# Kernel optimization log

Measured on AMD Instinct MI355X. Metric: run time of the kernel, lower is better.

The kernel has to match this reference:

```python
import jax, jax.numpy as jnp
import numpy as np

B = 16384
MOTION = 128      # motion_size
USED = 3          # used_motions
LAT = 32          # latent_size
H1 = 512
H2 = 512
MOE = 8
IN = MOTION * (USED - 1) + LAT  # 288 (used_angles = 0)


def setup_inputs() -> dict:
    key = jax.random.key(0)
    ks = jax.random.split(key, 14)
    s = 0.02
    return {
        "motions": jax.random.normal(ks[0], (B, MOTION * (USED - 1)), jnp.float32),
        "z": jax.random.normal(ks[1], (B, LAT), jnp.float32),
        # gate MLP params
        "gw1": jax.random.normal(ks[2], (IN, H1), jnp.float32) * s,
        "gb1": jnp.zeros((H1,), jnp.float32),
        "gw2": jax.random.normal(ks[3], (H1, H2), jnp.float32) * s,
        "gb2": jnp.zeros((H2,), jnp.float32),
        "gw3": jax.random.normal(ks[4], (H2, MOE), jnp.float32) * s,
        "gb3": jnp.zeros((MOE,), jnp.float32),
        # stacked expert params: layer k weight [MOE, in_k, out_k]
        "W1": jax.random.normal(ks[5], (MOE, IN, H1), jnp.float32) * s,
        "b1": jnp.zeros((MOE, H1), jnp.float32),
        "W2": jax.random.normal(ks[6], (MOE, H1 + LAT, H2), jnp.float32) * s,
        "b2": jnp.zeros((MOE, H2), jnp.float32),
        "W3": jax.random.normal(ks[7], (MOE, H2 + LAT, MOTION), jnp.float32) * s,
        "b3": jnp.zeros((MOE, MOTION), jnp.float32),
    }


def reference(motions, z, gw1, gb1, gw2, gb2, gw3, gb3, W1, b1, W2, b2, W3, b3):
    # used_angles == 0 -> angles is empty; input = concat([motions, z])
    x = jnp.concatenate([motions, z], axis=1)            # [B, IN]

    # gate: 3-layer ELU MLP -> per-expert blend weights [B, MOE]
    para = jax.nn.elu(x @ gw1 + gb1)
    para = jax.nn.elu(para @ gw2 + gb2)
    para = jax.nn.elu(para @ gw3 + gb3)

    # all experts batched via stacked weights (replaces Python loop)
    zb = jnp.broadcast_to(z[None], (MOE, B, LAT))        # z re-concatenated per layer
    h = jax.nn.elu(jnp.einsum('bi,eio->ebo', x, W1) + b1[:, None, :])              # [E,B,H1]
    h = jax.nn.elu(jnp.einsum('ebi,eio->ebo', jnp.concatenate([h, zb], -1), W2)
                   + b2[:, None, :])                                               # [E,B,H2]
    h = jax.nn.elu(jnp.einsum('ebi,eio->ebo', jnp.concatenate([h, zb], -1), W3)
                   + b3[:, None, :])                                               # [E,B,M]

    # gated combine, then divide by Frobenius norm of the whole gate matrix
    out = jnp.einsum('be,ebm->bm', para, h)              # [B, MOTION]
    out = out / jnp.linalg.norm(para)
    return jax.nn.sigmoid(out)
```

## Files before the change

kernel.cpp:

```cpp
#include <hip/hip_runtime.h>


typedef __attribute__((ext_vector_type(8))) short bf16x8;
typedef __attribute__((ext_vector_type(4))) float f32x4;
#define MFMA(a, b, c) __builtin_amdgcn_mfma_f32_16x16x32_bf16(a, b, c, 0, 0, 0)

#define STRIDE 552

__device__ __forceinline__ float elu_f(float x) { return x > 0.f ? x : (__expf(x) - 1.f); }

__device__ __forceinline__ ushort f2bf(float f) {
    union { float f; unsigned u; } v; v.f = f;
    unsigned r = v.u + 0x7fffu + ((v.u >> 16) & 1u);
    return (ushort)(r >> 16);
}
__device__ __forceinline__ float bf2f(ushort u) {
    union { unsigned u; float f; } v; v.u = ((unsigned)u) << 16;
    return v.f;
}
__device__ __forceinline__ bf16x8 ldg8(const ushort* p) { return *(const bf16x8*)p; }

__global__ void prep_xz(const float* __restrict__ motions, const float* __restrict__ z,
                        ushort* __restrict__ xz) {
    int i = blockIdx.x * 256 + threadIdx.x;
    int r = i / 72, c = i % 72;
    float4 v = (c < 64) ? ((const float4*)motions)[r * 64 + c]
                        : ((const float4*)z)[r * 8 + (c - 64)];
    ushort4 o;
    o.x = f2bf(v.x); o.y = f2bf(v.y); o.z = f2bf(v.z); o.w = f2bf(v.w);
    *(ushort4*)(xz + (size_t)r * 288 + c * 4) = o;
}

__global__ void prep_transpose(const float* __restrict__ in, ushort* __restrict__ out,
                               int K, int N) {
    __shared__ float tile[32][33];
    const int e = blockIdx.z;
    const float* inp = in + (size_t)e * K * N;
    ushort* outp = out + (size_t)e * N * K;
    const int k0 = blockIdx.x * 32, n0 = blockIdx.y * 32;
    const int tx = threadIdx.x, ty = threadIdx.y;
    #pragma unroll
    for (int i = 0; i < 4; ++i)
        tile[ty + i * 8][tx] = inp[(size_t)(k0 + ty + i * 8) * N + n0 + tx];
    __syncthreads();
    #pragma unroll
    for (int i = 0; i < 4; ++i)
        outp[(size_t)(n0 + ty + i * 8) * K + k0 + tx] = f2bf(tile[tx][ty + i * 8]);
}

__device__ __forceinline__ void layer_x288(
    int e, const ushort* __restrict__ Wall, const float* __restrict__ ball,
    const ushort* __restrict__ xrow, ushort* hdst, int n0, int lr, int lk)
{
    const ushort* Wt = Wall + (size_t)e * 512 * 288;
    f32x4 acc[4][2] = {};
    bf16x8 bc[2], bn[2];
    #pragma unroll
    for (int nf = 0; nf < 2; ++nf)
        bc[nf] = ldg8(Wt + (size_t)(n0 + nf * 16 + lr) * 288 + lk * 8);
    for (int ks = 0; ks < 9; ++ks) {
        if (ks < 8) {
            #pragma unroll
            for (int nf = 0; nf < 2; ++nf)
                bn[nf] = ldg8(Wt + (size_t)(n0 + nf * 16 + lr) * 288 + (ks + 1) * 32 + lk * 8);
        }
        bf16x8 a[4];
        #pragma unroll
        for (int mf = 0; mf < 4; ++mf)
            a[mf] = ldg8(xrow + (size_t)(mf * 16 + lr) * 288 + ks * 32 + lk * 8);
        #pragma unroll
        for (int mf = 0; mf < 4; ++mf) {
            acc[mf][0] = MFMA(bc[0], a[mf], acc[mf][0]);
            acc[mf][1] = MFMA(bc[1], a[mf], acc[mf][1]);
        }
        bc[0] = bn[0]; bc[1] = bn[1];
    }
    #pragma unroll
    for (int nf = 0; nf < 2; ++nf) {
        const int nb = n0 + nf * 16 + lk * 4;
        const float4 bb = *(const float4*)&ball[e * 512 + nb];
        #pragma unroll
        for (int mf = 0; mf < 4; ++mf) {
            const int row = mf * 16 + lr;
            ushort4 o;
            o.x = f2bf(elu_f(acc[mf][nf][0] + bb.x));
            o.y = f2bf(elu_f(acc[mf][nf][1] + bb.y));
            o.z = f2bf(elu_f(acc[mf][nf][2] + bb.z));
            o.w = f2bf(elu_f(acc[mf][nf][3] + bb.w));
            *(ushort4*)&hdst[row * STRIDE + nb] = o;
        }
    }
}

__device__ __forceinline__ void layer_h544(
    int e, const ushort* __restrict__ Wall, const float* __restrict__ ball,
    const ushort* hsrc, ushort* hdst, int n0, int lr, int lk)
{
    const ushort* Wt = Wall + (size_t)e * 512 * 544;
    f32x4 acc[4][2] = {};
    bf16x8 bc[2], bn[2];
    #pragma unroll
    for (int nf = 0; nf < 2; ++nf)
        bc[nf] = ldg8(Wt + (size_t)(n0 + nf * 16 + lr) * 544 + lk * 8);
    for (int ks = 0; ks < 17; ++ks) {
        if (ks < 16) {
            #pragma unroll
            for (int nf = 0; nf < 2; ++nf)
                bn[nf] = ldg8(Wt + (size_t)(n0 + nf * 16 + lr) * 544 + (ks + 1) * 32 + lk * 8);
        }
        bf16x8 a[4];
        #pragma unroll
        for (int mf = 0; mf < 4; ++mf)
            a[mf] = *(const bf16x8*)&hsrc[(mf * 16 + lr) * STRIDE + ks * 32 + lk * 8];
        #pragma unroll
        for (int mf = 0; mf < 4; ++mf) {
            acc[mf][0] = MFMA(bc[0], a[mf], acc[mf][0]);
            acc[mf][1] = MFMA(bc[1], a[mf], acc[mf][1]);
        }
        bc[0] = bn[0]; bc[1] = bn[1];
    }
    #pragma unroll
    for (int nf = 0; nf < 2; ++nf) {
        const int nb = n0 + nf * 16 + lk * 4;
        const float4 bb = *(const float4*)&ball[e * 512 + nb];
        #pragma unroll
        for (int mf = 0; mf < 4; ++mf) {
            const int row = mf * 16 + lr;
            ushort4 o;
            o.x = f2bf(elu_f(acc[mf][nf][0] + bb.x));
            o.y = f2bf(elu_f(acc[mf][nf][1] + bb.y));
            o.z = f2bf(elu_f(acc[mf][nf][2] + bb.z));
            o.w = f2bf(elu_f(acc[mf][nf][3] + bb.w));
            *(ushort4*)&hdst[row * STRIDE + nb] = o;
        }
    }
}

__global__ __launch_bounds__(1024, 1) void gate_kernel(
    const ushort* __restrict__ xz,
    const ushort* __restrict__ gw1t, const float* __restrict__ gb1,
    const ushort* __restrict__ gw2t, const float* __restrict__ gb2,
    const float* __restrict__ gw3, const float* __restrict__ gb3,
    float* __restrict__ para, float* __restrict__ partial)
{
    __shared__ ushort hs[64 * STRIDE];
    __shared__ float red[512];
    const int t = threadIdx.x;
    const int lane = t & 63, w = t >> 6;
    const int lr = lane & 15, lk = lane >> 4;
    const int r0 = blockIdx.x * 64;
    const ushort* xrow = xz + (size_t)r0 * 288;
    const int n0 = w * 32;

    {
        f32x4 acc[4][2] = {};
        bf16x8 bc[2], bn[2];
        #pragma unroll
        for (int nf = 0; nf < 2; ++nf)
            bc[nf] = ldg8(gw1t + (size_t)(n0 + nf * 16 + lr) * 288 + lk * 8);
        for (int ks = 0; ks < 9; ++ks) {
            if (ks < 8) {
                #pragma unroll
                for (int nf = 0; nf < 2; ++nf)
                    bn[nf] = ldg8(gw1t + (size_t)(n0 + nf * 16 + lr) * 288 + (ks + 1) * 32 + lk * 8);
            }
            bf16x8 a[4];
            #pragma unroll
            for (int mf = 0; mf < 4; ++mf)
                a[mf] = ldg8(xrow + (size_t)(mf * 16 + lr) * 288 + ks * 32 + lk * 8);
            #pragma unroll
            for (int mf = 0; mf < 4; ++mf) {
                acc[mf][0] = MFMA(bc[0], a[mf], acc[mf][0]);
                acc[mf][1] = MFMA(bc[1], a[mf], acc[mf][1]);
            }
            bc[0] = bn[0]; bc[1] = bn[1];
        }
        #pragma unroll
        for (int nf = 0; nf < 2; ++nf) {
            const int nb = n0 + nf * 16 + lk * 4;
            const float4 bb = *(const float4*)&gb1[nb];
            #pragma unroll
            for (int mf = 0; mf < 4; ++mf) {
                const int row = mf * 16 + lr;
                ushort4 o;
                o.x = f2bf(elu_f(acc[mf][nf][0] + bb.x));
                o.y = f2bf(elu_f(acc[mf][nf][1] + bb.y));
                o.z = f2bf(elu_f(acc[mf][nf][2] + bb.z));
                o.w = f2bf(elu_f(acc[mf][nf][3] + bb.w));
                *(ushort4*)&hs[row * STRIDE + nb] = o;
            }
        }
    }
    __syncthreads();

    {
        f32x4 acc[4][2] = {};
        bf16x8 bc[2], bn[2];
        #pragma unroll
        for (int nf = 0; nf < 2; ++nf)
            bc[nf] = ldg8(gw2t + (size_t)(n0 + nf * 16 + lr) * 512 + lk * 8);
        for (int ks = 0; ks < 16; ++ks) {
            if (ks < 15) {
                #pragma unroll
                for (int nf = 0; nf < 2; ++nf)
                    bn[nf] = ldg8(gw2t + (size_t)(n0 + nf * 16 + lr) * 512 + (ks + 1) * 32 + lk * 8);
            }
            bf16x8 a[4];
            #pragma unroll
            for (int mf = 0; mf < 4; ++mf)
                a[mf] = *(const bf16x8*)&hs[(mf * 16 + lr) * STRIDE + ks * 32 + lk * 8];
            #pragma unroll
            for (int mf = 0; mf < 4; ++mf) {
                acc[mf][0] = MFMA(bc[0], a[mf], acc[mf][0]);
                acc[mf][1] = MFMA(bc[1], a[mf], acc[mf][1]);
            }
            bc[0] = bn[0]; bc[1] = bn[1];
        }
        __syncthreads();
        #pragma unroll
        for (int nf = 0; nf < 2; ++nf) {
            const int nb = n0 + nf * 16 + lk * 4;
            const float4 bb = *(const float4*)&gb2[nb];
            #pragma unroll
            for (int mf = 0; mf < 4; ++mf) {
                const int row = mf * 16 + lr;
                ushort4 o;
                o.x = f2bf(elu_f(acc[mf][nf][0] + bb.x));
                o.y = f2bf(elu_f(acc[mf][nf][1] + bb.y));
                o.z = f2bf(elu_f(acc[mf][nf][2] + bb.z));
                o.w = f2bf(elu_f(acc[mf][nf][3] + bb.w));
                *(ushort4*)&hs[row * STRIDE + nb] = o;
            }
        }
    }
    __syncthreads();

    if (t < 512) {
        const int row = t >> 3, e = t & 7;
        float acc = 0.f;
        for (int k = 0; k < 512; k += 8) {
            uint4 hv = *(const uint4*)&hs[row * STRIDE + k];
            acc += bf2f((ushort)(hv.x)) * gw3[(k + 0) * 8 + e];
            acc += bf2f((ushort)(hv.x >> 16)) * gw3[(k + 1) * 8 + e];
            acc += bf2f((ushort)(hv.y)) * gw3[(k + 2) * 8 + e];
            acc += bf2f((ushort)(hv.y >> 16)) * gw3[(k + 3) * 8 + e];
            acc += bf2f((ushort)(hv.z)) * gw3[(k + 4) * 8 + e];
            acc += bf2f((ushort)(hv.z >> 16)) * gw3[(k + 5) * 8 + e];
            acc += bf2f((ushort)(hv.w)) * gw3[(k + 6) * 8 + e];
            acc += bf2f((ushort)(hv.w >> 16)) * gw3[(k + 7) * 8 + e];
        }
        float p = elu_f(acc + gb3[e]);
        para[(size_t)(r0 + row) * 8 + e] = p;
        red[t] = p * p;
    }
    __syncthreads();
    for (int s = 256; s >= 1; s >>= 1) {
        if (t < s) red[t] += red[t + s];
        __syncthreads();
    }
    if (t == 0) partial[blockIdx.x] = red[0];
}

__global__ void finalize_kernel(const float* __restrict__ partial, float* __restrict__ invn) {
    __shared__ float red[256];
    const int t = threadIdx.x;
    red[t] = partial[t];
    __syncthreads();
    for (int s = 128; s >= 1; s >>= 1) {
        if (t < s) red[t] += red[t + s];
        __syncthreads();
    }
    if (t == 0) invn[0] = 1.0f / sqrtf(red[0]);
}

__global__ __launch_bounds__(1024, 1) void expert_kernel(
    const ushort* __restrict__ xz, const float* __restrict__ z,
    const ushort* __restrict__ W1t, const float* __restrict__ b1,
    const ushort* __restrict__ W2t, const float* __restrict__ b2,
    const ushort* __restrict__ W3t, const float* __restrict__ b3,
    const float* __restrict__ para, const float* __restrict__ invn,
    float* __restrict__ out)
{
    __shared__ ushort hA[64 * STRIDE];
    __shared__ ushort hB[64 * STRIDE];
    __shared__ float ps[64 * 8];
    const int t = threadIdx.x;
    const int lane = t & 63, w = t >> 6;
    const int lr = lane & 15, lk = lane >> 4;
    const int r0 = blockIdx.x * 64;
    const ushort* xrow = xz + (size_t)r0 * 288;
    const int n0 = w * 32;
    const int rb = (w >> 2) * 16;
    const int c0 = (w & 3) * 32;

    for (int i = t; i < 2048; i += 1024) {
        int r = i >> 5, c = i & 31;
        ushort v = f2bf(z[(size_t)(r0 + r) * 32 + c]);
        hA[r * STRIDE + 512 + c] = v;
        hB[r * STRIDE + 512 + c] = v;
    }
    if (t < 512) ps[t] = para[(size_t)r0 * 8 + t];
    const float inv_norm = invn[0];

    f32x4 oacc[2] = {};

    layer_x288(0, W1t, b1, xrow, hA, n0, lr, lk);
    __syncthreads();

    for (int e = 0; e < 8; ++e) {
        layer_h544(e, W2t, b2, hA, hB, n0, lr, lk);
        __syncthreads();

        {
            const ushort* Wt = W3t + (size_t)e * 128 * 544;
            f32x4 acc3[2] = {};
            bf16x8 bc[2], bn[2];
            #pragma unroll
            for (int nf = 0; nf < 2; ++nf)
                bc[nf] = ldg8(Wt + (size_t)(c0 + nf * 16 + lr) * 544 + lk * 8);
            for (int ks = 0; ks < 17; ++ks) {
                if (ks < 16) {
                    #pragma unroll
                    for (int nf = 0; nf < 2; ++nf)
                        bn[nf] = ldg8(Wt + (size_t)(c0 + nf * 16 + lr) * 544 + (ks + 1) * 32 + lk * 8);
                }
                bf16x8 a = *(const bf16x8*)&hB[(rb + lr) * STRIDE + ks * 32 + lk * 8];
                acc3[0] = MFMA(bc[0], a, acc3[0]);
                acc3[1] = MFMA(bc[1], a, acc3[1]);
                bc[0] = bn[0]; bc[1] = bn[1];
            }
            const float pse = ps[(rb + lr) * 8 + e];
            #pragma unroll
            for (int nf = 0; nf < 2; ++nf) {
                const float4 bb = *(const float4*)&b3[e * 128 + c0 + nf * 16 + lk * 4];
                oacc[nf][0] += pse * elu_f(acc3[nf][0] + bb.x);
                oacc[nf][1] += pse * elu_f(acc3[nf][1] + bb.y);
                oacc[nf][2] += pse * elu_f(acc3[nf][2] + bb.z);
                oacc[nf][3] += pse * elu_f(acc3[nf][3] + bb.w);
            }
        }
        if (e < 7)
            layer_x288(e + 1, W1t, b1, xrow, hA, n0, lr, lk);
        __syncthreads();
    }

    #pragma unroll
    for (int nf = 0; nf < 2; ++nf) {
        float4 o;
        o.x = 1.0f / (1.0f + __expf(-oacc[nf][0] * inv_norm));
        o.y = 1.0f / (1.0f + __expf(-oacc[nf][1] * inv_norm));
        o.z = 1.0f / (1.0f + __expf(-oacc[nf][2] * inv_norm));
        o.w = 1.0f / (1.0f + __expf(-oacc[nf][3] * inv_norm));
        *(float4*)&out[(size_t)(r0 + rb + lr) * 128 + c0 + nf * 16 + lk * 4] = o;
    }
}

extern "C" void kernel_launch(void* const* d_in, const int* in_sizes, int n_in,
                              void* d_out, int out_size, void* d_ws, size_t ws_size,
                              hipStream_t stream) {
    const float* motions = (const float*)d_in[0];
    const float* z   = (const float*)d_in[1];
    const float* gw1 = (const float*)d_in[2];
    const float* gb1 = (const float*)d_in[3];
    const float* gw2 = (const float*)d_in[4];
    const float* gb2 = (const float*)d_in[5];
    const float* gw3 = (const float*)d_in[6];
    const float* gb3 = (const float*)d_in[7];
    const float* W1  = (const float*)d_in[8];
    const float* b1  = (const float*)d_in[9];
    const float* W2  = (const float*)d_in[10];
    const float* b2  = (const float*)d_in[11];
    const float* W3  = (const float*)d_in[12];
    const float* b3  = (const float*)d_in[13];
    float* out = (float*)d_out;

    char* W = (char*)d_ws;
    ushort* xz      = (ushort*)(W);
    ushort* gw1t    = (ushort*)(W + 9437184);
    ushort* gw2t    = (ushort*)(W + 9732096);
    ushort* W1t     = (ushort*)(W + 10256384);
    ushort* W2t     = (ushort*)(W + 12615680);
    ushort* W3t     = (ushort*)(W + 17072128);
    float*  para    = (float*) (W + 18186240);
    float*  partial = (float*) (W + 18710528);
    float*  invn    = (float*) (W + 18711552);

    prep_xz<<<dim3(4608), dim3(256), 0, stream>>>(motions, z, xz);
    prep_transpose<<<dim3(9, 16, 1), dim3(32, 8), 0, stream>>>(gw1, gw1t, 288, 512);
    prep_transpose<<<dim3(16, 16, 1), dim3(32, 8), 0, stream>>>(gw2, gw2t, 512, 512);
    prep_transpose<<<dim3(9, 16, 8), dim3(32, 8), 0, stream>>>(W1, W1t, 288, 512);
    prep_transpose<<<dim3(17, 16, 8), dim3(32, 8), 0, stream>>>(W2, W2t, 544, 512);
    prep_transpose<<<dim3(17, 4, 8), dim3(32, 8), 0, stream>>>(W3, W3t, 544, 128);

    gate_kernel<<<dim3(256), dim3(1024), 0, stream>>>(xz, gw1t, gb1, gw2t, gb2, gw3, gb3,
                                                      para, partial);
    finalize_kernel<<<dim3(1), dim3(256), 0, stream>>>(partial, invn);
    expert_kernel<<<dim3(256), dim3(1024), 0, stream>>>(xz, z, W1t, b1, W2t, b2, W3t, b3,
                                                        para, invn, out);
}
```

Baseline: 340.8 us.

## Shrink expert tile to 32 rows, single LDS buffer, two blocks per CU

The expert kernel now processes 32 rows per block with 512 threads instead of 64 rows with 1024. Each wave covers 64 output columns with 4 N-fragments, and the two activation buffers are merged into one LDS buffer, using an extra barrier before the in-place overwrite. Halving LDS use per block lets two blocks share a CU, which should raise occupancy and let one block's barriers and global weight loads overlap with the other's MFMA work. In exchange, weights are reused across half as many rows per load, so global and L2 weight traffic per output row roughly doubles, and the overlap of the next expert's layer 1 with layer 3 is dropped.

Measured after the change: 427.0 us. 1.25x slower.

```diff
diff --git a/kernel.cpp b/kernel.cpp
--- a/kernel.cpp
+++ b/kernel.cpp
@@ -46,94 +46,6 @@
     #pragma unroll
     for (int i = 0; i < 4; ++i)
         outp[(size_t)(n0 + ty + i * 8) * K + k0 + tx] = f2bf(tile[tx][ty + i * 8]);
-}
-
-__device__ __forceinline__ void layer_x288(
-    int e, const ushort* __restrict__ Wall, const float* __restrict__ ball,
-    const ushort* __restrict__ xrow, ushort* hdst, int n0, int lr, int lk)
-{
-    const ushort* Wt = Wall + (size_t)e * 512 * 288;
-    f32x4 acc[4][2] = {};
-    bf16x8 bc[2], bn[2];
-    #pragma unroll
-    for (int nf = 0; nf < 2; ++nf)
-        bc[nf] = ldg8(Wt + (size_t)(n0 + nf * 16 + lr) * 288 + lk * 8);
-    for (int ks = 0; ks < 9; ++ks) {
-        if (ks < 8) {
-            #pragma unroll
-            for (int nf = 0; nf < 2; ++nf)
-                bn[nf] = ldg8(Wt + (size_t)(n0 + nf * 16 + lr) * 288 + (ks + 1) * 32 + lk * 8);
-        }
-        bf16x8 a[4];
-        #pragma unroll
-        for (int mf = 0; mf < 4; ++mf)
-            a[mf] = ldg8(xrow + (size_t)(mf * 16 + lr) * 288 + ks * 32 + lk * 8);
-        #pragma unroll
-        for (int mf = 0; mf < 4; ++mf) {
-            acc[mf][0] = MFMA(bc[0], a[mf], acc[mf][0]);
-            acc[mf][1] = MFMA(bc[1], a[mf], acc[mf][1]);
-        }
-        bc[0] = bn[0]; bc[1] = bn[1];
-    }
-    #pragma unroll
-    for (int nf = 0; nf < 2; ++nf) {
-        const int nb = n0 + nf * 16 + lk * 4;
-        const float4 bb = *(const float4*)&ball[e * 512 + nb];
-        #pragma unroll
-        for (int mf = 0; mf < 4; ++mf) {
-            const int row = mf * 16 + lr;
-            ushort4 o;
-            o.x = f2bf(elu_f(acc[mf][nf][0] + bb.x));
-            o.y = f2bf(elu_f(acc[mf][nf][1] + bb.y));
-            o.z = f2bf(elu_f(acc[mf][nf][2] + bb.z));
-            o.w = f2bf(elu_f(acc[mf][nf][3] + bb.w));
-            *(ushort4*)&hdst[row * STRIDE + nb] = o;
-        }
-    }
-}
-
-__device__ __forceinline__ void layer_h544(
-    int e, const ushort* __restrict__ Wall, const float* __restrict__ ball,
-    const ushort* hsrc, ushort* hdst, int n0, int lr, int lk)
-{
-    const ushort* Wt = Wall + (size_t)e * 512 * 544;
-    f32x4 acc[4][2] = {};
-    bf16x8 bc[2], bn[2];
-    #pragma unroll
-    for (int nf = 0; nf < 2; ++nf)
-        bc[nf] = ldg8(Wt + (size_t)(n0 + nf * 16 + lr) * 544 + lk * 8);
-    for (int ks = 0; ks < 17; ++ks) {
-        if (ks < 16) {
-            #pragma unroll
-            for (int nf = 0; nf < 2; ++nf)
-                bn[nf] = ldg8(Wt + (size_t)(n0 + nf * 16 + lr) * 544 + (ks + 1) * 32 + lk * 8);
-        }
-        bf16x8 a[4];
-        #pragma unroll
-        for (int mf = 0; mf < 4; ++mf)
-            a[mf] = *(const bf16x8*)&hsrc[(mf * 16 + lr) * STRIDE + ks * 32 + lk * 8];
-        #pragma unroll
-        for (int mf = 0; mf < 4; ++mf) {
-            acc[mf][0] = MFMA(bc[0], a[mf], acc[mf][0]);
-            acc[mf][1] = MFMA(bc[1], a[mf], acc[mf][1]);
-        }
-        bc[0] = bn[0]; bc[1] = bn[1];
-    }
-    #pragma unroll
-    for (int nf = 0; nf < 2; ++nf) {
-        const int nb = n0 + nf * 16 + lk * 4;
-        const float4 bb = *(const float4*)&ball[e * 512 + nb];
-        #pragma unroll
-        for (int mf = 0; mf < 4; ++mf) {
-            const int row = mf * 16 + lr;
-            ushort4 o;
-            o.x = f2bf(elu_f(acc[mf][nf][0] + bb.x));
-            o.y = f2bf(elu_f(acc[mf][nf][1] + bb.y));
-            o.z = f2bf(elu_f(acc[mf][nf][2] + bb.z));
-            o.w = f2bf(elu_f(acc[mf][nf][3] + bb.w));
-            *(ushort4*)&hdst[row * STRIDE + nb] = o;
-        }
-    }
 }
 
 __global__ __launch_bounds__(1024, 1) void gate_kernel(
@@ -273,7 +185,7 @@
     if (t == 0) invn[0] = 1.0f / sqrtf(red[0]);
 }
 
-__global__ __launch_bounds__(1024, 1) void expert_kernel(
+__global__ __launch_bounds__(512, 2) void expert_kernel(
     const ushort* __restrict__ xz, const float* __restrict__ z,
     const ushort* __restrict__ W1t, const float* __restrict__ b1,
     const ushort* __restrict__ W2t, const float* __restrict__ b2,
@@ -281,34 +193,110 @@
     const float* __restrict__ para, const float* __restrict__ invn,
     float* __restrict__ out)
 {
-    __shared__ ushort hA[64 * STRIDE];
-    __shared__ ushort hB[64 * STRIDE];
-    __shared__ float ps[64 * 8];
+    __shared__ ushort hs[32 * STRIDE];
+    __shared__ float ps[32 * 8];
     const int t = threadIdx.x;
     const int lane = t & 63, w = t >> 6;
     const int lr = lane & 15, lk = lane >> 4;
-    const int r0 = blockIdx.x * 64;
+    const int r0 = blockIdx.x * 32;
     const ushort* xrow = xz + (size_t)r0 * 288;
-    const int n0 = w * 32;
+    const int n0 = w * 64;
     const int rb = (w >> 2) * 16;
     const int c0 = (w & 3) * 32;
 
-    for (int i = t; i < 2048; i += 1024) {
+    for (int i = t; i < 1024; i += 512) {
         int r = i >> 5, c = i & 31;
-        ushort v = f2bf(z[(size_t)(r0 + r) * 32 + c]);
-        hA[r * STRIDE + 512 + c] = v;
-        hB[r * STRIDE + 512 + c] = v;
-    }
-    if (t < 512) ps[t] = para[(size_t)r0 * 8 + t];
+        hs[r * STRIDE + 512 + c] = f2bf(z[(size_t)(r0 + r) * 32 + c]);
+    }
+    if (t < 256) ps[t] = para[(size_t)r0 * 8 + t];
     const float inv_norm = invn[0];
 
     f32x4 oacc[2] = {};
 
-    layer_x288(0, W1t, b1, xrow, hA, n0, lr, lk);
-    __syncthreads();
-
     for (int e = 0; e < 8; ++e) {
-        layer_h544(e, W2t, b2, hA, hB, n0, lr, lk);
+        __syncthreads();
+
+        {
+            const ushort* Wt = W1t + (size_t)e * 512 * 288;
+            f32x4 acc[2][4] = {};
+            bf16x8 bc[4], bn[4];
+            #pragma unroll
+            for (int nf = 0; nf < 4; ++nf)
+                bc[nf] = ldg8(Wt + (size_t)(n0 + nf * 16 + lr) * 288 + lk * 8);
+            for (int ks = 0; ks < 9; ++ks) {
+                if (ks < 8) {
+                    #pragma unroll
+                    for (int nf = 0; nf < 4; ++nf)
+                        bn[nf] = ldg8(Wt + (size_t)(n0 + nf * 16 + lr) * 288 + (ks + 1) * 32 + lk * 8);
+                }
+                #pragma unroll
+                for (int mf = 0; mf < 2; ++mf) {
+                    bf16x8 a = ldg8(xrow + (size_t)(mf * 16 + lr) * 288 + ks * 32 + lk * 8);
+                    #pragma unroll
+                    for (int nf = 0; nf < 4; ++nf)
+                        acc[mf][nf] = MFMA(bc[nf], a, acc[mf][nf]);
+                }
+                #pragma unroll
+                for (int nf = 0; nf < 4; ++nf) bc[nf] = bn[nf];
+            }
+            #pragma unroll
+            for (int nf = 0; nf < 4; ++nf) {
+                const int nb = n0 + nf * 16 + lk * 4;
+                const float4 bb = *(const float4*)&b1[e * 512 + nb];
+                #pragma unroll
+                for (int mf = 0; mf < 2; ++mf) {
+                    const int row = mf * 16 + lr;
+                    ushort4 o;
+                    o.x = f2bf(elu_f(acc[mf][nf][0] + bb.x));
+                    o.y = f2bf(elu_f(acc[mf][nf][1] + bb.y));
+                    o.z = f2bf(elu_f(acc[mf][nf][2] + bb.z));
+                    o.w = f2bf(elu_f(acc[mf][nf][3] + bb.w));
+                    *(ushort4*)&hs[row * STRIDE + nb] = o;
+                }
+            }
+        }
+        __syncthreads();
+
+        {
+            const ushort* Wt = W2t + (size_t)e * 512 * 544;
+            f32x4 acc[2][4] = {};
+            bf16x8 bc[4], bn[4];
+            #pragma unroll
+            for (int nf = 0; nf < 4; ++nf)
+                bc[nf] = ldg8(Wt + (size_t)(n0 + nf * 16 + lr) * 544 + lk * 8);
+            for (int ks = 0; ks < 17; ++ks) {
+                if (ks < 16) {
+                    #pragma unroll
+                    for (int nf = 0; nf < 4; ++nf)
+                        bn[nf] = ldg8(Wt + (size_t)(n0 + nf * 16 + lr) * 544 + (ks + 1) * 32 + lk * 8);
+                }
+                #pragma unroll
+                for (int mf = 0; mf < 2; ++mf) {
+                    bf16x8 a = *(const bf16x8*)&hs[(mf * 16 + lr) * STRIDE + ks * 32 + lk * 8];
+                    #pragma unroll
+                    for (int nf = 0; nf < 4; ++nf)
+                        acc[mf][nf] = MFMA(bc[nf], a, acc[mf][nf]);
+                }
+                #pragma unroll
+                for (int nf = 0; nf < 4; ++nf) bc[nf] = bn[nf];
+            }
+            __syncthreads();
+            #pragma unroll
+            for (int nf = 0; nf < 4; ++nf) {
+                const int nb = n0 + nf * 16 + lk * 4;
+                const float4 bb = *(const float4*)&b2[e * 512 + nb];
+                #pragma unroll
+                for (int mf = 0; mf < 2; ++mf) {
+                    const int row = mf * 16 + lr;
+                    ushort4 o;
+                    o.x = f2bf(elu_f(acc[mf][nf][0] + bb.x));
+                    o.y = f2bf(elu_f(acc[mf][nf][1] + bb.y));
+                    o.z = f2bf(elu_f(acc[mf][nf][2] + bb.z));
+                    o.w = f2bf(elu_f(acc[mf][nf][3] + bb.w));
+                    *(ushort4*)&hs[row * STRIDE + nb] = o;
+                }
+            }
+        }
         __syncthreads();
 
         {
@@ -324,7 +312,7 @@
                     for (int nf = 0; nf < 2; ++nf)
                         bn[nf] = ldg8(Wt + (size_t)(c0 + nf * 16 + lr) * 544 + (ks + 1) * 32 + lk * 8);
                 }
-                bf16x8 a = *(const bf16x8*)&hB[(rb + lr) * STRIDE + ks * 32 + lk * 8];
+                bf16x8 a = *(const bf16x8*)&hs[(rb + lr) * STRIDE + ks * 32 + lk * 8];
                 acc3[0] = MFMA(bc[0], a, acc3[0]);
                 acc3[1] = MFMA(bc[1], a, acc3[1]);
                 bc[0] = bn[0]; bc[1] = bn[1];
@@ -339,9 +327,6 @@
                 oacc[nf][3] += pse * elu_f(acc3[nf][3] + bb.w);
             }
         }
-        if (e < 7)
-            layer_x288(e + 1, W1t, b1, xrow, hA, n0, lr, lk);
-        __syncthreads();
     }
 
     #pragma unroll
@@ -395,6 +380,6 @@
     gate_kernel<<<dim3(256), dim3(1024), 0, stream>>>(xz, gw1t, gb1, gw2t, gb2, gw3, gb3,
                                                       para, partial);
     finalize_kernel<<<dim3(1), dim3(256), 0, stream>>>(partial, invn);
-    expert_kernel<<<dim3(256), dim3(1024), 0, stream>>>(xz, z, W1t, b1, W2t, b2, W3t, b3,
-                                                        para, invn, out);
-}
+    expert_kernel<<<dim3(512), dim3(512), 0, stream>>>(xz, z, W1t, b1, W2t, b2, W3t, b3,
+                                                       para, invn, out);
+}
```
